# Performance work log

Hardware: AMD Instinct MI355X
Metric: run time of the kernel (lower is better)

Reference implementation:

```python
import jax, jax.numpy as jnp
import numpy as np

B, T, H, V, NT, NH, DFF = 2, 512, 768, 51865, 3, 4, 2048
EPS = 1e-5


def setup_inputs() -> dict:
    key = jax.random.key(0)
    ks = jax.random.split(key, 24)
    s = 0.02
    d = {
        "encoder_hidden": jax.random.normal(ks[0], (B, T, H), jnp.float32),
        "teacher_tokens": jax.random.randint(ks[1], (B, T, NT), 0, V, jnp.int32),
        "start_token": jax.random.normal(ks[2], (1, H), jnp.float32),
        "emb": jax.random.normal(ks[3], (V, H), jnp.float32) * s,
        # self-attention (torch MultiheadAttention packed qkv in_proj)
        "sa_in_w": jax.random.normal(ks[4], (3 * H, H), jnp.float32) * s,
        "sa_in_b": jnp.zeros((3 * H,), jnp.float32),
        "sa_out_w": jax.random.normal(ks[5], (H, H), jnp.float32) * s,
        "sa_out_b": jnp.zeros((H,), jnp.float32),
        # cross-attention
        "ca_in_w": jax.random.normal(ks[6], (3 * H, H), jnp.float32) * s,
        "ca_in_b": jnp.zeros((3 * H,), jnp.float32),
        "ca_out_w": jax.random.normal(ks[7], (H, H), jnp.float32) * s,
        "ca_out_b": jnp.zeros((H,), jnp.float32),
        # FFN
        "lin1_w": jax.random.normal(ks[8], (DFF, H), jnp.float32) * s,
        "lin1_b": jnp.zeros((DFF,), jnp.float32),
        "lin2_w": jax.random.normal(ks[9], (H, DFF), jnp.float32) * s,
        "lin2_b": jnp.zeros((H,), jnp.float32),
        # layer norms (post-norm TransformerDecoderLayer)
        "ln1_g": jnp.ones((H,), jnp.float32), "ln1_b": jnp.zeros((H,), jnp.float32),
        "ln2_g": jnp.ones((H,), jnp.float32), "ln2_b": jnp.zeros((H,), jnp.float32),
        "ln3_g": jnp.ones((H,), jnp.float32), "ln3_b": jnp.zeros((H,), jnp.float32),
        # output vocab projection (bias=False)
        "proj_w": jax.random.normal(ks[10], (V, H), jnp.float32) * s,
    }
    return d


def _ln(x, g, b):
    m = jnp.mean(x, -1, keepdims=True)
    v = jnp.mean(jnp.square(x - m), -1, keepdims=True)
    return (x - m) * jax.lax.rsqrt(v + EPS) * g + b


def _mha(xq, xkv, in_w, in_b, out_w, out_b, mask=None):
    # xq: (N, Lq, H), xkv: (N, Lk, H). torch packed in_proj: [Wq; Wk; Wv].
    h = xq.shape[-1]
    wq, wk, wv = jnp.split(in_w, 3, axis=0)
    bq, bk, bv = jnp.split(in_b, 3, axis=0)
    hd = h // NH
    q = (xq @ wq.T + bq).reshape(*xq.shape[:-1], NH, hd)
    k = (xkv @ wk.T + bk).reshape(*xkv.shape[:-1], NH, hd)
    v = (xkv @ wv.T + bv).reshape(*xkv.shape[:-1], NH, hd)
    scores = jnp.einsum("nqhd,nkhd->nhqk", q, k) / jnp.sqrt(jnp.float32(hd)).astype(q.dtype)
    if mask is not None:
        scores = scores + mask  # (Lq,Lk) additive causal mask
    a = jax.nn.softmax(scores, axis=-1)
    o = jnp.einsum("nhqk,nkhd->nqhd", a, v).reshape(*xq.shape[:-1], h)
    return o @ out_w.T + out_b


def _forward(encoder_hidden, teacher_tokens, start_token, emb,
             sa_in_w, sa_in_b, sa_out_w, sa_out_b,
             ca_in_w, ca_in_b, ca_out_w, ca_out_b,
             lin1_w, lin1_b, lin2_w, lin2_b,
             ln1_g, ln1_b, ln2_g, ln2_b, ln3_g, ln3_b, proj_w):
    b, t, h = encoder_hidden.shape
    nt = teacher_tokens.shape[-1]
    n = b * t
    # With teacher forcing + causal mask, step-i logits == position-i output of a
    # single decoder pass over [start, emb(teacher[..., :nt-1])] with memory of length 1.
    tok_emb = jnp.take(emb, teacher_tokens[:, :, : nt - 1], axis=0)  # (B,T,NT-1,H)
    start = jnp.broadcast_to(start_token.reshape(1, 1, 1, h), (b, t, 1, h))
    tgt = jnp.concatenate([start, tok_emb], axis=2).reshape(n, nt, h)  # (N,NT,H)
    mem = encoder_hidden.reshape(n, 1, h)  # (N,1,H)
    causal = jnp.where(jnp.triu(jnp.ones((nt, nt), bool), 1), -jnp.inf, 0.0).astype(tgt.dtype)
    # post-norm TransformerDecoderLayer (dropout=identity at eval)
    x = tgt
    x = _ln(x + _mha(x, x, sa_in_w, sa_in_b, sa_out_w, sa_out_b, causal), ln1_g, ln1_b)
    x = _ln(x + _mha(x, mem, ca_in_w, ca_in_b, ca_out_w, ca_out_b), ln2_g, ln2_b)
    ff = jax.nn.relu(x @ lin1_w.T + lin1_b) @ lin2_w.T + lin2_b
    x = _ln(x + ff, ln3_g, ln3_b)
    logits = x @ proj_w.T  # (N,NT,V)
    return logits.reshape(b, t, nt, -1)


def reference(encoder_hidden, teacher_tokens, start_token, emb,
              sa_in_w, sa_in_b, sa_out_w, sa_out_b,
              ca_in_w, ca_in_b, ca_out_w, ca_out_b,
              lin1_w, lin1_b, lin2_w, lin2_b,
              ln1_g, ln1_b, ln2_g, ln2_b, ln3_g, ln3_b, proj_w):
    return _forward(encoder_hidden, teacher_tokens, start_token, emb,
                    sa_in_w, sa_in_b, sa_out_w, sa_out_b,
                    ca_in_w, ca_in_b, ca_out_w, ca_out_b,
                    lin1_w, lin1_b, lin2_w, lin2_b,
                    ln1_g, ln1_b, ln2_g, ln2_b, ln3_g, ln3_b, proj_w)
```

## Files before the change

kernel.cpp:

```cpp
#include <hip/hip_runtime.h>

typedef __bf16 bf16;
typedef __bf16 bf16x4 __attribute__((ext_vector_type(4)));
typedef __bf16 bf16x8 __attribute__((ext_vector_type(8)));
typedef float f32x4 __attribute__((ext_vector_type(4)));

#define BM 128
#define BN 128
#define BK 32

__device__ __forceinline__ void async16(const void* g, void* l) {
    __builtin_amdgcn_global_load_lds(
        (__attribute__((address_space(1))) void*)g,
        (__attribute__((address_space(3))) void*)l,
        16, 0, 0);
}

__global__ __launch_bounds__(512, 2) void gemm8p(
    const bf16* __restrict__ A, const bf16* __restrict__ W,
    float* __restrict__ C, int K, int ldo, int Nstore, int nTilesM)
{
    __shared__ bf16 lds[2][32768];

    int nwg = gridDim.x;
    int orig = blockIdx.x;
    int q = nwg >> 3, r = nwg & 7, xcd = orig & 7, local = orig >> 3;
    int wgid = (xcd < r ? xcd * (q + 1) : r * (q + 1) + (xcd - r) * q) + local;
    const int brow = (wgid % nTilesM) * 256;
    const int bcol = (wgid / nTilesM) * 256;

    const int t = threadIdx.x;
    const int wid = t >> 6, lane = t & 63;
    const int wm = wid >> 2, wn = wid & 3;
    const int l15 = lane & 15, l7 = lane & 7, lhi = lane >> 4;

    const int lr = t >> 3;
    const int cc = (t & 7) ^ (lr & 7);
    const bf16* gA = A + (size_t)(brow + lr) * K + cc * 8;
    const bf16* gW = W + (size_t)(bcol + lr) * K + cc * 8;
    const int dsto = wid * 512;

    const int kx0 = ((0 * 4 + lhi) ^ l7) * 8;
    const int kx1 = ((1 * 4 + lhi) ^ l7) * 8;
    const int abase = wm * 8192 + l15 * 64;
    const int bbase = 16384 + (wn >> 1) * 8192 + ((wn & 1) * 64 + l15) * 64;

    f32x4 acc[8][4] = {};
    const int nkt = K >> 6;

    #define ST_A(dst, k0)                                             \
        async16(gA + (k0),                   (dst) + dsto);           \
        async16(gA + (size_t)64 * K + (k0),  (dst) + 4096 + dsto);    \
        async16(gA + (size_t)128 * K + (k0), (dst) + 8192 + dsto);    \
        async16(gA + (size_t)192 * K + (k0), (dst) + 12288 + dsto);
    #define ST_B(dst, k0)                                                     \
        async16(gW + (k0),                   (dst) + 16384 + dsto);           \
        async16(gW + (size_t)64 * K + (k0),  (dst) + 20480 + dsto);           \
        async16(gW + (size_t)128 * K + (k0), (dst) + 24576 + dsto);           \
        async16(gW + (size_t)192 * K + (k0), (dst) + 28672 + dsto);

    { ST_A(&lds[0][0], 0); ST_B(&lds[0][0], 0); }

    bf16x8 a[4][2], b[4][2];
    for (int kt = 0; kt < nkt; ++kt) {
        const bf16* cur = &lds[kt & 1][0];
        bf16* stg = &lds[(kt + 1) & 1][0];
        const int k1 = (kt + 1) << 6;
        const bool st = (kt + 1 < nkt);

        if (st) { ST_A(stg, k1); }
        if (st) asm volatile("s_waitcnt vmcnt(4)" ::: "memory");
        else    asm volatile("s_waitcnt vmcnt(0)" ::: "memory");
        __builtin_amdgcn_s_barrier();
        #pragma unroll
        for (int fi = 0; fi < 4; fi++) {
            a[fi][0] = *(const bf16x8*)(cur + abase + fi * 1024 + kx0);
            a[fi][1] = *(const bf16x8*)(cur + abase + fi * 1024 + kx1);
        }
        #pragma unroll
        for (int fj = 0; fj < 4; fj++) {
            b[fj][0] = *(const bf16x8*)(cur + bbase + fj * 1024 + kx0);
            b[fj][1] = *(const bf16x8*)(cur + bbase + fj * 1024 + kx1);
        }
        if (st) { ST_B(stg, k1); }
        __builtin_amdgcn_s_setprio(1);
        #pragma unroll
        for (int fi = 0; fi < 4; fi++)
            #pragma unroll
            for (int fj = 0; fj < 4; fj++) {
                f32x4 c0 = acc[fi][fj];
                c0 = __builtin_amdgcn_mfma_f32_16x16x32_bf16(a[fi][0], b[fj][0], c0, 0,0,0);
                c0 = __builtin_amdgcn_mfma_f32_16x16x32_bf16(a[fi][1], b[fj][1], c0, 0,0,0);
                acc[fi][fj] = c0;
            }
        __builtin_amdgcn_s_setprio(0);

        #pragma unroll
        for (int fi = 0; fi < 4; fi++) {
            a[fi][0] = *(const bf16x8*)(cur + abase + 4096 + fi * 1024 + kx0);
            a[fi][1] = *(const bf16x8*)(cur + abase + 4096 + fi * 1024 + kx1);
        }
        __builtin_amdgcn_s_setprio(1);
        #pragma unroll
        for (int fi = 0; fi < 4; fi++)
            #pragma unroll
            for (int fj = 0; fj < 2; fj++) {
                f32x4 c0 = acc[4 + fi][fj];
                c0 = __builtin_amdgcn_mfma_f32_16x16x32_bf16(a[fi][0], b[fj][0], c0, 0,0,0);
                c0 = __builtin_amdgcn_mfma_f32_16x16x32_bf16(a[fi][1], b[fj][1], c0, 0,0,0);
                acc[4 + fi][fj] = c0;
            }
        __builtin_amdgcn_s_setprio(0);
        __builtin_amdgcn_s_barrier();
        __builtin_amdgcn_s_setprio(1);
        #pragma unroll
        for (int fi = 0; fi < 4; fi++)
            #pragma unroll
            for (int fj = 2; fj < 4; fj++) {
                f32x4 c0 = acc[4 + fi][fj];
                c0 = __builtin_amdgcn_mfma_f32_16x16x32_bf16(a[fi][0], b[fj][0], c0, 0,0,0);
                c0 = __builtin_amdgcn_mfma_f32_16x16x32_bf16(a[fi][1], b[fj][1], c0, 0,0,0);
                acc[4 + fi][fj] = c0;
            }
        __builtin_amdgcn_s_setprio(0);
    }
    #undef ST_A
    #undef ST_B

    float* ldsf = (float*)&lds[0][0];
    const int lhi4 = lhi * 4;
    #pragma unroll
    for (int h = 0; h < 2; h++) {
        if (h) __builtin_amdgcn_s_barrier();
        #pragma unroll
        for (int fi4 = 0; fi4 < 4; fi4++) {
            #pragma unroll
            for (int fj = 0; fj < 4; fj++) {
                f32x4 v = acc[h * 4 + fi4][fj];
                int row0 = wm * 64 + fi4 * 16 + lhi4;
                int col = wn * 64 + fj * 16 + l15;
                #pragma unroll
                for (int r2 = 0; r2 < 4; r2++) {
                    int row = row0 + r2;
                    ldsf[row * 256 + (col ^ ((row & 12) << 1))] = v[r2];
                }
            }
        }
        __builtin_amdgcn_s_barrier();
        #pragma unroll
        for (int i = 0; i < 16; i++) {
            int c = i * 512 + t;
            int row = c >> 6, ch = c & 63;
            f32x4 v = *(const f32x4*)(ldsf + row * 256
                                      + ((ch ^ ((row & 12) >> 1)) << 2));
            int grow = brow + (row >> 6) * 128 + h * 64 + (row & 63);
            int gcol = bcol + ch * 4;
            float* dst = C + (size_t)grow * ldo + gcol;
            if (gcol + 4 <= Nstore) {
                __builtin_nontemporal_store(v, (f32x4*)dst);
            } else {
                #pragma unroll
                for (int k2 = 0; k2 < 4; k2++)
                    if (gcol + k2 < Nstore) dst[k2] = v[k2];
            }
        }
    }
}

__global__ __launch_bounds__(256) void gemm_bt(
    const bf16* __restrict__ A, const bf16* __restrict__ W,
    const float* __restrict__ bias,
    float* __restrict__ outF, bf16* __restrict__ outB,
    int M, int K, int ldo, int Nstore, int relu)
{
    __shared__ bf16 As[2][4096];
    __shared__ bf16 Ws[2][4096];
    const int brow = blockIdx.y * BM;
    const int bcol = blockIdx.x * BN;
    const int t = threadIdx.x;
    const int wv = t >> 6;
    const int lane = t & 63;
    const int wrow = (wv >> 1) * 64;
    const int wcol = (wv & 1) * 64;

    f32x4 acc[4][4] = {};

    const int row0 = t >> 2;
    const int cg = (t & 3) * 8;
    const bf16* gA = A + (size_t)(brow + row0) * K + cg;
    const bf16* gW = W + (size_t)(bcol + row0) * K + cg;
    const size_t rstep = (size_t)64 * K;
    const int dsto = wv * 512;

    const int lrow = lane & 15;
    const int kg = (lane >> 4) * 8;

    #define ST(buf, k0)                                   \
        async16(gA + (k0), &As[buf][0] + dsto);           \
        async16(gA + rstep + (k0), &As[buf][2048] + dsto);\
        async16(gW + (k0), &Ws[buf][0] + dsto);           \
        async16(gW + rstep + (k0), &Ws[buf][2048] + dsto);

    const int nkt = K >> 5;
    ST(0, 0);
    for (int kt = 0; kt < nkt; ++kt) {
        const int cur = kt & 1;
        if (kt + 1 < nkt) {
            ST(cur ^ 1, (kt + 1) << 5);
            asm volatile("s_waitcnt vmcnt(4)" ::: "memory");
        } else {
            asm volatile("s_waitcnt vmcnt(0)" ::: "memory");
        }
        __builtin_amdgcn_s_barrier();
        bf16x8 af[4], wf[4];
        #pragma unroll
        for (int i = 0; i < 4; i++)
            af[i] = *(const bf16x8*)(&As[cur][0] + (wrow + i * 16 + lrow) * BK + kg);
        #pragma unroll
        for (int j = 0; j < 4; j++)
            wf[j] = *(const bf16x8*)(&Ws[cur][0] + (wcol + j * 16 + lrow) * BK + kg);
        __builtin_amdgcn_s_setprio(1);
        #pragma unroll
        for (int i = 0; i < 4; i++)
            #pragma unroll
            for (int j = 0; j < 4; j++)
                acc[i][j] = __builtin_amdgcn_mfma_f32_16x16x32_bf16(
                    af[i], wf[j], acc[i][j], 0, 0, 0);
        __builtin_amdgcn_s_setprio(0);
        __builtin_amdgcn_s_barrier();
    }
    #undef ST

    const int lcol = lane & 15;
    const int rb = (lane >> 4) * 4;
    #pragma unroll
    for (int j = 0; j < 4; j++) {
        int n = bcol + wcol + j * 16 + lcol;
        if (n >= Nstore) continue;
        float bv = bias ? bias[n] : 0.f;
        #pragma unroll
        for (int i = 0; i < 4; i++) {
            #pragma unroll
            for (int r = 0; r < 4; r++) {
                int m = brow + wrow + i * 16 + rb + r;
                float v = acc[i][j][r] + bv;
                if (relu) v = fmaxf(v, 0.f);
                size_t off = (size_t)m * ldo + n;
                if (outF) outF[off] = v;
                if (outB) outB[off] = (bf16)v;
            }
        }
    }
}

__global__ __launch_bounds__(256) void cvt_bf16(
    const float* __restrict__ in, bf16* __restrict__ out,
    size_t nvalid, size_t ntotal)
{
    size_t i = ((size_t)blockIdx.x * 256 + threadIdx.x) * 4;
    if (i >= ntotal) return;
    bf16x4 r;
    if (i < nvalid) {
        f32x4 f = __builtin_nontemporal_load((const f32x4*)(in + i));
        r[0] = (bf16)f[0]; r[1] = (bf16)f[1]; r[2] = (bf16)f[2]; r[3] = (bf16)f[3];
    } else {
        r[0] = (bf16)0.f; r[1] = (bf16)0.f; r[2] = (bf16)0.f; r[3] = (bf16)0.f;
    }
    *(bf16x4*)(out + i) = r;
}

__global__ __launch_bounds__(256) void build_tgt(
    const float* __restrict__ start, const float* __restrict__ emb,
    const int* __restrict__ toks, float* __restrict__ outF, bf16* __restrict__ outB)
{
    int r = blockIdx.x;
    int n = r / 3, p = r % 3;
    const float* src = (p == 0) ? start : emb + (size_t)toks[n * 3 + (p - 1)] * 768;
    int t = threadIdx.x;
    #pragma unroll
    for (int j = 0; j < 3; j++) {
        int c = t + j * 256;
        float v = src[c];
        outF[(size_t)r * 768 + c] = v;
        outB[(size_t)r * 768 + c] = (bf16)v;
    }
}

__global__ __launch_bounds__(64) void attn3(
    const float* __restrict__ qkv, bf16* __restrict__ o)
{
    int blk = blockIdx.x;
    int n = blk >> 2, h = blk & 3;
    int lane = threadIdx.x;
    const float* base = qkv + (size_t)n * 3 * 2304 + h * 192;
    float q[3][3], k[3][3], v[3][3];
    #pragma unroll
    for (int p = 0; p < 3; p++)
        #pragma unroll
        for (int j = 0; j < 3; j++) {
            int d = lane + j * 64;
            q[p][j] = base[p * 2304 + d];
            k[p][j] = base[p * 2304 + 768 + d];
            v[p][j] = base[p * 2304 + 1536 + d];
        }
    float s[3][3];
    #pragma unroll
    for (int p = 0; p < 3; p++)
        #pragma unroll
        for (int pk = 0; pk < 3; pk++) {
            if (pk > p) continue;
            float ps = q[p][0] * k[pk][0] + q[p][1] * k[pk][1] + q[p][2] * k[pk][2];
            #pragma unroll
            for (int off = 32; off; off >>= 1) ps += __shfl_xor(ps, off);
            s[p][pk] = ps * 0.072168783648703220563f;
        }
    float a[3][3] = {};
    a[0][0] = 1.f;
    {
        float m = fmaxf(s[1][0], s[1][1]);
        float e0 = expf(s[1][0] - m), e1 = expf(s[1][1] - m);
        float inv = 1.f / (e0 + e1);
        a[1][0] = e0 * inv; a[1][1] = e1 * inv;
    }
    {
        float m = fmaxf(fmaxf(s[2][0], s[2][1]), s[2][2]);
        float e0 = expf(s[2][0] - m), e1 = expf(s[2][1] - m), e2 = expf(s[2][2] - m);
        float inv = 1.f / (e0 + e1 + e2);
        a[2][0] = e0 * inv; a[2][1] = e1 * inv; a[2][2] = e2 * inv;
    }
    bf16* ob = o + (size_t)n * 3 * 768 + h * 192;
    #pragma unroll
    for (int p = 0; p < 3; p++)
        #pragma unroll
        for (int j = 0; j < 3; j++) {
            float val = a[p][0] * v[0][j];
            if (p >= 1) val += a[p][1] * v[1][j];
            if (p >= 2) val += a[p][2] * v[2][j];
            ob[p * 768 + lane + j * 64] = (bf16)val;
        }
}

__global__ __launch_bounds__(256) void add_ln(
    const float* __restrict__ a, const float* __restrict__ b,
    const float* __restrict__ g, const float* __restrict__ be,
    float* __restrict__ outF, bf16* __restrict__ outB, int bcast)
{
    int r = blockIdx.x;
    int t = threadIdx.x;
    const float* ar = a + (size_t)r * 768;
    const float* br = b + (size_t)(bcast ? (r / 3) : r) * 768;
    float x[3];
    float s = 0.f, sq = 0.f;
    #pragma unroll
    for (int j = 0; j < 3; j++) {
        int c = t + j * 256;
        x[j] = ar[c] + br[c];
        s += x[j]; sq += x[j] * x[j];
    }
    #pragma unroll
    for (int off = 32; off; off >>= 1) {
        s += __shfl_xor(s, off);
        sq += __shfl_xor(sq, off);
    }
    __shared__ float ls[4], lq[4];
    int wv = t >> 6;
    if ((t & 63) == 0) { ls[wv] = s; lq[wv] = sq; }
    __syncthreads();
    s = ls[0] + ls[1] + ls[2] + ls[3];
    sq = lq[0] + lq[1] + lq[2] + lq[3];
    float mean = s * (1.f / 768.f);
    float var = sq * (1.f / 768.f) - mean * mean;
    float inv = rsqrtf(var + 1e-5f);
    #pragma unroll
    for (int j = 0; j < 3; j++) {
        int c = t + j * 256;
        float y = (x[j] - mean) * inv * g[c] + be[c];
        if (outF) outF[(size_t)r * 768 + c] = y;
        if (outB) outB[(size_t)r * 768 + c] = (bf16)y;
    }
}

static inline void run_gemm(const bf16* A, const bf16* W, const float* bias,
                            float* outF, bf16* outB, int M, int Npad, int K,
                            int ldo, int Nstore, int relu, hipStream_t s)
{
    dim3 grid(Npad / BN, M / BM);
    gemm_bt<<<grid, 256, 0, s>>>(A, W, bias, outF, outB, M, K, ldo, Nstore, relu);
}

static inline void run_cvt(const float* in, bf16* out, size_t nvalid,
                           size_t ntotal, hipStream_t s)
{
    int blocks = (int)((ntotal / 4 + 255) / 256);
    cvt_bf16<<<blocks, 256, 0, s>>>(in, out, nvalid, ntotal);
}

extern "C" void kernel_launch(void* const* d_in, const int* in_sizes, int n_in,
                              void* d_out, int out_size, void* d_ws, size_t ws_size,
                              hipStream_t stream)
{
    const float* enc      = (const float*)d_in[0];
    const int*   toks     = (const int*)d_in[1];
    const float* start    = (const float*)d_in[2];
    const float* emb      = (const float*)d_in[3];
    const float* sa_in_w  = (const float*)d_in[4];
    const float* sa_in_b  = (const float*)d_in[5];
    const float* sa_out_w = (const float*)d_in[6];
    const float* sa_out_b = (const float*)d_in[7];
    const float* ca_in_w  = (const float*)d_in[8];
    const float* ca_in_b  = (const float*)d_in[9];
    const float* ca_out_w = (const float*)d_in[10];
    const float* ca_out_b = (const float*)d_in[11];
    const float* lin1_w   = (const float*)d_in[12];
    const float* lin1_b   = (const float*)d_in[13];
    const float* lin2_w   = (const float*)d_in[14];
    const float* lin2_b   = (const float*)d_in[15];
    const float* ln1_g    = (const float*)d_in[16];
    const float* ln1_bb   = (const float*)d_in[17];
    const float* ln2_g    = (const float*)d_in[18];
    const float* ln2_bb   = (const float*)d_in[19];
    const float* ln3_g    = (const float*)d_in[20];
    const float* ln3_bb   = (const float*)d_in[21];
    const float* proj_w   = (const float*)d_in[22];
    float* out = (float*)d_out;

    const int NTOK = 3072;
    const int NM   = 1024;
    const int H    = 768;
    const int V    = 51865;
    const int VPAD = 51968;
    const int DFF  = 2048;

    char* p = (char*)d_ws;
    auto alloc = [&](size_t bytes) {
        void* r = (void*)p;
        p += (bytes + 255) & ~(size_t)255;
        return r;
    };
    float* tgt_f = (float*)alloc((size_t)NTOK * H * 4);
    float* x1_f  = (float*)alloc((size_t)NTOK * H * 4);
    float* x2_f  = (float*)alloc((size_t)NTOK * H * 4);
    float* big_f = (float*)alloc((size_t)NTOK * 2304 * 4);
    bf16*  actA  = (bf16*)alloc((size_t)NTOK * 2304 * 2);
    bf16*  actB  = (bf16*)alloc((size_t)NTOK * DFF * 2);
    bf16*  Wbf   = (bf16*)alloc((size_t)VPAD * H * 2);
    bf16*  mem_bf = actB;
    bf16*  v_bf   = actB + (size_t)NM * H;
    float* cao_f  = big_f + (size_t)NTOK * H;

    build_tgt<<<NTOK, 256, 0, stream>>>(start, emb, toks, tgt_f, actA);

    run_cvt(sa_in_w, Wbf, (size_t)2304 * H, (size_t)2304 * H, stream);
    run_gemm(actA, Wbf, sa_in_b, big_f, nullptr, NTOK, 2304, H, 2304, 2304, 0, stream);

    attn3<<<NM * 4, 64, 0, stream>>>(big_f, actA);

    run_cvt(sa_out_w, Wbf, (size_t)H * H, (size_t)H * H, stream);
    run_gemm(actA, Wbf, sa_out_b, big_f, nullptr, NTOK, H, H, H, H, 0, stream);

    add_ln<<<NTOK, 256, 0, stream>>>(tgt_f, big_f, ln1_g, ln1_bb, x1_f, nullptr, 0);

    run_cvt(enc, mem_bf, (size_t)NM * H, (size_t)NM * H, stream);
    run_cvt(ca_in_w + (size_t)1536 * H, Wbf, (size_t)H * H, (size_t)H * H, stream);
    run_gemm(mem_bf, Wbf, ca_in_b + 1536, nullptr, v_bf, NM, H, H, H, H, 0, stream);
    run_cvt(ca_out_w, Wbf, (size_t)H * H, (size_t)H * H, stream);
    run_gemm(v_bf, Wbf, ca_out_b, cao_f, nullptr, NM, H, H, H, H, 0, stream);

    add_ln<<<NTOK, 256, 0, stream>>>(x1_f, cao_f, ln2_g, ln2_bb, x2_f, actA, 1);

    run_cvt(lin1_w, Wbf, (size_t)DFF * H, (size_t)DFF * H, stream);
    run_gemm(actA, Wbf, lin1_b, nullptr, actB, NTOK, DFF, H, DFF, DFF, 1, stream);

    run_cvt(lin2_w, Wbf, (size_t)H * DFF, (size_t)H * DFF, stream);
    run_gemm(actB, Wbf, lin2_b, big_f, nullptr, NTOK, H, DFF, H, H, 0, stream);

    add_ln<<<NTOK, 256, 0, stream>>>(x2_f, big_f, ln3_g, ln3_bb, nullptr, actA, 0);

    run_cvt(proj_w, Wbf, (size_t)V * H, (size_t)VPAD * H, stream);
    {
        dim3 grid((NTOK / 256) * (VPAD / 256));
        gemm8p<<<grid, 512, 0, stream>>>(actA, Wbf, out, H, V, V, NTOK / 256);
    }
}
```

Measured before the change: 552.2 us.

## Restructure GEMM main loop into 8-phase ping-pong schedule with split async loads

Rewrites the K-loop of the 256x256 bf16 MFMA GEMM so each iteration handles two K-tiles. The work is split into eight phases that alternate quarter-tile MFMA blocks with half-sized async global-to-LDS loads, separated by barriers. The aim is to interleave memory traffic with compute more finely, in the style of HipKittens-type 8-wave ping-pong schedules. It adds many more barriers and assumes nkt is even. If K/64 is odd, the final tile is skipped.

```diff
diff --git a/kernel.cpp b/kernel.cpp
--- a/kernel.cpp
+++ b/kernel.cpp
@@ -40,92 +40,145 @@
     const bf16* gW = W + (size_t)(bcol + lr) * K + cc * 8;
     const int dsto = wid * 512;
 
-    const int kx0 = ((0 * 4 + lhi) ^ l7) * 8;
-    const int kx1 = ((1 * 4 + lhi) ^ l7) * 8;
+    const int kx0 = (lhi ^ l7) * 8;
+    const int kx1 = ((4 + lhi) ^ l7) * 8;
     const int abase = wm * 8192 + l15 * 64;
     const int bbase = 16384 + (wn >> 1) * 8192 + ((wn & 1) * 64 + l15) * 64;
 
     f32x4 acc[8][4] = {};
     const int nkt = K >> 6;
 
-    #define ST_A(dst, k0)                                             \
-        async16(gA + (k0),                   (dst) + dsto);           \
-        async16(gA + (size_t)64 * K + (k0),  (dst) + 4096 + dsto);    \
-        async16(gA + (size_t)128 * K + (k0), (dst) + 8192 + dsto);    \
-        async16(gA + (size_t)192 * K + (k0), (dst) + 12288 + dsto);
-    #define ST_B(dst, k0)                                                     \
-        async16(gW + (k0),                   (dst) + 16384 + dsto);           \
-        async16(gW + (size_t)64 * K + (k0),  (dst) + 20480 + dsto);           \
-        async16(gW + (size_t)128 * K + (k0), (dst) + 24576 + dsto);           \
-        async16(gW + (size_t)192 * K + (k0), (dst) + 28672 + dsto);
-
-    { ST_A(&lds[0][0], 0); ST_B(&lds[0][0], 0); }
-
-    bf16x8 a[4][2], b[4][2];
-    for (int kt = 0; kt < nkt; ++kt) {
-        const bf16* cur = &lds[kt & 1][0];
-        bf16* stg = &lds[(kt + 1) & 1][0];
-        const int k1 = (kt + 1) << 6;
-        const bool st = (kt + 1 < nkt);
-
-        if (st) { ST_A(stg, k1); }
-        if (st) asm volatile("s_waitcnt vmcnt(4)" ::: "memory");
-        else    asm volatile("s_waitcnt vmcnt(0)" ::: "memory");
+    #define SA0(d, k0) { async16(gA + (k0), (d) + dsto); \
+                         async16(gA + (size_t)64*K + (k0), (d) + 4096 + dsto); }
+    #define SA1(d, k0) { async16(gA + (size_t)128*K + (k0), (d) + 8192 + dsto); \
+                         async16(gA + (size_t)192*K + (k0), (d) + 12288 + dsto); }
+    #define SB0(d, k0) { async16(gW + (k0), (d) + 16384 + dsto); \
+                         async16(gW + (size_t)64*K + (k0), (d) + 20480 + dsto); }
+    #define SB1(d, k0) { async16(gW + (size_t)128*K + (k0), (d) + 24576 + dsto); \
+                         async16(gW + (size_t)192*K + (k0), (d) + 28672 + dsto); }
+
+    bf16* b0 = &lds[0][0];
+    bf16* b1 = &lds[1][0];
+
+    SA0(b0, 0) SA1(b0, 0) SB0(b0, 0) SB1(b0, 0)
+    SA0(b1, 64) SA1(b1, 64)
+
+    bf16x8 a0[4][2], a1[4][2], b[4][2];
+    const int niter = nkt >> 1;
+
+    #define MFMA16(QM, QN, AR)                                                  \
+        __builtin_amdgcn_s_setprio(1);                                          \
+        _Pragma("unroll")                                                       \
+        for (int fi = 0; fi < 4; fi++)                                          \
+            _Pragma("unroll")                                                   \
+            for (int fj = 0; fj < 2; fj++) {                                    \
+                f32x4 c0 = acc[(QM)*4 + fi][(QN)*2 + fj];                       \
+                c0 = __builtin_amdgcn_mfma_f32_16x16x32_bf16(                   \
+                        AR[fi][0], b[(QN)*2 + fj][0], c0, 0, 0, 0);             \
+                c0 = __builtin_amdgcn_mfma_f32_16x16x32_bf16(                   \
+                        AR[fi][1], b[(QN)*2 + fj][1], c0, 0, 0, 0);             \
+                acc[(QM)*4 + fi][(QN)*2 + fj] = c0;                             \
+            }                                                                   \
+        __builtin_amdgcn_s_setprio(0);
+
+    for (int it = 0; it < niter; ++it) {
+        const int kO  = (2 * it + 1) << 6;
+        const int kE2 = (2 * it + 2) << 6;
+        const int kO2 = (2 * it + 3) << 6;
+        const bool sE2 = (2 * it + 2) < nkt;
+        const bool sO2 = (2 * it + 3) < nkt;
+
+        SB0(b1, kO)
+        asm volatile("s_waitcnt vmcnt(6)" ::: "memory");
         __builtin_amdgcn_s_barrier();
         #pragma unroll
         for (int fi = 0; fi < 4; fi++) {
-            a[fi][0] = *(const bf16x8*)(cur + abase + fi * 1024 + kx0);
-            a[fi][1] = *(const bf16x8*)(cur + abase + fi * 1024 + kx1);
-        }
-        #pragma unroll
-        for (int fj = 0; fj < 4; fj++) {
-            b[fj][0] = *(const bf16x8*)(cur + bbase + fj * 1024 + kx0);
-            b[fj][1] = *(const bf16x8*)(cur + bbase + fj * 1024 + kx1);
-        }
-        if (st) { ST_B(stg, k1); }
-        __builtin_amdgcn_s_setprio(1);
-        #pragma unroll
-        for (int fi = 0; fi < 4; fi++)
-            #pragma unroll
-            for (int fj = 0; fj < 4; fj++) {
-                f32x4 c0 = acc[fi][fj];
-                c0 = __builtin_amdgcn_mfma_f32_16x16x32_bf16(a[fi][0], b[fj][0], c0, 0,0,0);
-                c0 = __builtin_amdgcn_mfma_f32_16x16x32_bf16(a[fi][1], b[fj][1], c0, 0,0,0);
-                acc[fi][fj] = c0;
-            }
-        __builtin_amdgcn_s_setprio(0);
+            a0[fi][0] = *(const bf16x8*)(b0 + abase + fi * 1024 + kx0);
+            a0[fi][1] = *(const bf16x8*)(b0 + abase + fi * 1024 + kx1);
+        }
+        #pragma unroll
+        for (int fj = 0; fj < 2; fj++) {
+            b[fj][0] = *(const bf16x8*)(b0 + bbase + fj * 1024 + kx0);
+            b[fj][1] = *(const bf16x8*)(b0 + bbase + fj * 1024 + kx1);
+        }
+        MFMA16(0, 0, a0)
+        __builtin_amdgcn_s_barrier();
 
         #pragma unroll
         for (int fi = 0; fi < 4; fi++) {
-            a[fi][0] = *(const bf16x8*)(cur + abase + 4096 + fi * 1024 + kx0);
-            a[fi][1] = *(const bf16x8*)(cur + abase + 4096 + fi * 1024 + kx1);
-        }
-        __builtin_amdgcn_s_setprio(1);
-        #pragma unroll
-        for (int fi = 0; fi < 4; fi++)
-            #pragma unroll
-            for (int fj = 0; fj < 2; fj++) {
-                f32x4 c0 = acc[4 + fi][fj];
-                c0 = __builtin_amdgcn_mfma_f32_16x16x32_bf16(a[fi][0], b[fj][0], c0, 0,0,0);
-                c0 = __builtin_amdgcn_mfma_f32_16x16x32_bf16(a[fi][1], b[fj][1], c0, 0,0,0);
-                acc[4 + fi][fj] = c0;
-            }
-        __builtin_amdgcn_s_setprio(0);
-        __builtin_amdgcn_s_barrier();
-        __builtin_amdgcn_s_setprio(1);
-        #pragma unroll
-        for (int fi = 0; fi < 4; fi++)
-            #pragma unroll
-            for (int fj = 2; fj < 4; fj++) {
-                f32x4 c0 = acc[4 + fi][fj];
-                c0 = __builtin_amdgcn_mfma_f32_16x16x32_bf16(a[fi][0], b[fj][0], c0, 0,0,0);
-                c0 = __builtin_amdgcn_mfma_f32_16x16x32_bf16(a[fi][1], b[fj][1], c0, 0,0,0);
-                acc[4 + fi][fj] = c0;
-            }
-        __builtin_amdgcn_s_setprio(0);
-    }
-    #undef ST_A
-    #undef ST_B
+            a1[fi][0] = *(const bf16x8*)(b0 + abase + 4096 + fi * 1024 + kx0);
+            a1[fi][1] = *(const bf16x8*)(b0 + abase + 4096 + fi * 1024 + kx1);
+        }
+        #pragma unroll
+        for (int fj = 2; fj < 4; fj++) {
+            b[fj][0] = *(const bf16x8*)(b0 + bbase + fj * 1024 + kx0);
+            b[fj][1] = *(const bf16x8*)(b0 + bbase + fj * 1024 + kx1);
+        }
+        SB1(b1, kO)
+        __builtin_amdgcn_s_barrier();
+        MFMA16(1, 0, a1)
+        __builtin_amdgcn_s_barrier();
+
+        if (sE2) { SA0(b0, kE2) }
+        __builtin_amdgcn_s_barrier();
+        MFMA16(1, 1, a1)
+        __builtin_amdgcn_s_barrier();
+
+        if (sE2) { SA1(b0, kE2) }
+        __builtin_amdgcn_s_barrier();
+        MFMA16(0, 1, a0)
+        __builtin_amdgcn_s_barrier();
+
+        if (sE2) {
+            SB0(b0, kE2)
+            asm volatile("s_waitcnt vmcnt(6)" ::: "memory");
+        } else {
+            asm volatile("s_waitcnt vmcnt(0)" ::: "memory");
+        }
+        __builtin_amdgcn_s_barrier();
+        #pragma unroll
+        for (int fi = 0; fi < 4; fi++) {
+            a0[fi][0] = *(const bf16x8*)(b1 + abase + fi * 1024 + kx0);
+            a0[fi][1] = *(const bf16x8*)(b1 + abase + fi * 1024 + kx1);
+        }
+        #pragma unroll
+        for (int fj = 0; fj < 2; fj++) {
+            b[fj][0] = *(const bf16x8*)(b1 + bbase + fj * 1024 + kx0);
+            b[fj][1] = *(const bf16x8*)(b1 + bbase + fj * 1024 + kx1);
+        }
+        MFMA16(0, 0, a0)
+        __builtin_amdgcn_s_barrier();
+
+        #pragma unroll
+        for (int fi = 0; fi < 4; fi++) {
+            a1[fi][0] = *(const bf16x8*)(b1 + abase + 4096 + fi * 1024 + kx0);
+            a1[fi][1] = *(const bf16x8*)(b1 + abase + 4096 + fi * 1024 + kx1);
+        }
+        #pragma unroll
+        for (int fj = 2; fj < 4; fj++) {
+            b[fj][0] = *(const bf16x8*)(b1 + bbase + fj * 1024 + kx0);
+            b[fj][1] = *(const bf16x8*)(b1 + bbase + fj * 1024 + kx1);
+        }
+        if (sE2) { SB1(b0, kE2) }
+        __builtin_amdgcn_s_barrier();
+        MFMA16(1, 0, a1)
+        __builtin_amdgcn_s_barrier();
+
+        if (sO2) { SA0(b1, kO2) }
+        __builtin_amdgcn_s_barrier();
+        MFMA16(1, 1, a1)
+        __builtin_amdgcn_s_barrier();
+
+        if (sO2) { SA1(b1, kO2) }
+        __builtin_amdgcn_s_barrier();
+        MFMA16(0, 1, a0)
+        __builtin_amdgcn_s_barrier();
+    }
+    #undef MFMA16
+    #undef SA0
+    #undef SA1
+    #undef SB0
+    #undef SB1
 
     float* ldsf = (float*)&lds[0][0];
     const int lhi4 = lhi * 4;
```

New measurement: 755.0 us. 1.37x slower.
